# Performance work log

Hardware: AMD Instinct MI355X
Metric: run time of the kernel (lower is better)

The kernel has to match this reference:

```python
import jax, jax.numpy as jnp
import numpy as np

DIM = 768
NUM_EXPERTS = 4
NUM_HEADS = 12
HEAD_DIM = DIM // NUM_HEADS
MLP_HID = 4 * DIM
FC1_OUT = MLP_HID + 3 * DIM   # 5376 (mlp hidden + qkv)
FC2_IN = MLP_HID + DIM        # 3840 (mlp hidden + attn out)
FC2_OUT = 2 * DIM             # 1536 (mlp out + attn proj out)
CAP_FACTOR = 0.5
LN_EPS = 1e-6


def setup_inputs() -> dict:
    key = jax.random.key(0)
    ks = jax.random.split(key, 4)
    B, N = 8, 1024
    return {
        "x": jax.random.normal(ks[0], (B, N, DIM), jnp.float32),
        "w_router": jax.random.normal(ks[1], (NUM_EXPERTS, DIM), jnp.float32) * 0.02,
        "gamma1": jnp.ones((DIM,), jnp.float32),
        "beta1": jnp.zeros((DIM,), jnp.float32),
        "w1": jax.random.normal(ks[2], (FC1_OUT, DIM), jnp.float32) * 0.02,
        "b1": jnp.zeros((FC1_OUT,), jnp.float32),
        "w2": jax.random.normal(ks[3], (FC2_OUT, FC2_IN), jnp.float32) * 0.02,
        "b2": jnp.zeros((FC2_OUT,), jnp.float32),
    }


def reference(x, w_router, gamma1, beta1, w1, b1, w2, b2):
    B, N, C = x.shape
    E = NUM_EXPERTS
    cap = int(CAP_FACTOR * N)
    # nested (MoNE) per-expert active dims: [96, 192, 384, 768] for E=4, C=768
    m = np.array([C // 2 ** (E - 1 - e) for e in range(E)])
    in_mask = (np.arange(C)[None, :] < m[:, None]).astype(np.float32)  # [E, C]
    in_mask = jnp.asarray(in_mask)
    out_mask = jnp.concatenate([in_mask, in_mask], axis=-1)  # [E, 2C] for fc2 chunks

    # ---- expert-choice router ----
    logits = jnp.einsum('bnc,ec->bne', x, w_router)          # [B, N, E]
    probs = jax.nn.softmax(logits, axis=-1)
    gate, idx = jax.lax.top_k(jnp.swapaxes(probs, 1, 2), cap)  # [B, E, cap]
    dispatch = jax.nn.one_hot(idx, N, dtype=x.dtype)           # [B, E, cap, N]
    combine = dispatch * gate[..., None]                       # [B, E, cap, N]

    # ---- norm1 ----
    mu = jnp.mean(x, -1, keepdims=True)
    var = jnp.var(x, -1, keepdims=True)
    y = (x - mu) * jax.lax.rsqrt(var + LN_EPS) * gamma1 + beta1

    # ---- experts_choose_masked_contract (fc1, nested input dims) ----
    xg = jnp.einsum('becn,bnd->becd', dispatch, y)             # gather [B,E,cap,C]
    xg = xg * in_mask[None, :, None, :]                        # nested expert slice
    h = jnp.einsum('becd,fd->becf', xg, w1) + b1               # [B,E,cap,FC1_OUT]
    h = jnp.einsum('becn,becf->bnf', dispatch, h)              # scatter [B,N,FC1_OUT]

    x_mlp, x_qkv = h[..., :MLP_HID], h[..., MLP_HID:]

    # ---- attention ----
    qkv = x_qkv.reshape(B, N, 3, NUM_HEADS, HEAD_DIM).transpose(2, 0, 3, 1, 4)
    q, k, v = qkv[0], qkv[1], qkv[2]                           # [B,H,N,hd]
    scale = HEAD_DIM ** -0.5
    attn = jax.nn.softmax(jnp.einsum('bhqd,bhkd->bhqk', q, k) * scale, axis=-1)
    x_attn = jnp.einsum('bhqk,bhkd->bhqd', attn, v)
    x_attn = x_attn.transpose(0, 2, 1, 3).reshape(B, N, C)

    # ---- mlp activation + concat ----
    x_mlp = jax.nn.gelu(x_mlp, approximate=False)
    y2 = jnp.concatenate([x_mlp, x_attn], axis=-1)             # [B,N,FC2_IN]

    # ---- experts_choose_masked_expand (fc2, nested output dims, combine-weighted) ----
    yg = jnp.einsum('becn,bnf->becf', dispatch, y2)            # gather [B,E,cap,FC2_IN]
    o = jnp.einsum('becf,of->beco', yg, w2) + b2               # [B,E,cap,FC2_OUT]
    o = o * out_mask[None, :, None, :]                         # nested expert output slice
    z = jnp.einsum('becn,beco->bno', combine, o)               # combine [B,N,FC2_OUT]

    x_mlp2, x_attn2 = z[..., :C], z[..., C:]
    return x + x_mlp2 + x_attn2
```

## Files before the change

### kernel.cpp

```cpp
#include <hip/hip_runtime.h>
#include <math.h>

typedef __bf16 bf16_t;
typedef __bf16 bf16x8 __attribute__((ext_vector_type(8)));
typedef __bf16 bf16x4 __attribute__((ext_vector_type(4)));
typedef float f32x4 __attribute__((ext_vector_type(4)));

#define DIM 768
#define NE 4
#define NH 12
#define HD 64
#define MLP_HID 3072
#define FC1_OUT 5376
#define FC2_IN 3840
#define CAP 512
#define LOG2E 1.44269504088896340736f

__device__ __forceinline__ void async_copy16(const void* g, void* l) {
  __builtin_amdgcn_global_load_lds((const __attribute__((address_space(1))) void*)g,
                                   (__attribute__((address_space(3))) void*)l, 16, 0, 0);
}

__device__ __forceinline__ float gelu_f(float v) {
  float v2 = v * v;
  float t = v * fmaf(-0.102944f, v2, -2.302208f);
  float e = exp2f(t);
  return v * __builtin_amdgcn_rcpf(1.0f + e);
}

__global__ __launch_bounds__(256) void cast_router_kernel(const float* __restrict__ w1,
                                                          const float* __restrict__ w2,
                                                          bf16_t* __restrict__ w1b,
                                                          bf16_t* __restrict__ w2b,
                                                          const float* __restrict__ x,
                                                          const float* __restrict__ wr,
                                                          float* __restrict__ probs) {
  if (blockIdx.x < 2048) {
    const int N1 = FC1_OUT * DIM / 4;
    const int N2 = 1536 * FC2_IN / 4;
    const float4* w1v = (const float4*)w1;
    const float4* w2v = (const float4*)w2;
    for (int i = blockIdx.x * 256 + threadIdx.x; i < N1 + N2; i += 2048 * 256) {
      float4 f;
      bf16_t* dst;
      if (i < N1) { f = w1v[i]; dst = w1b + (size_t)i * 4; }
      else        { f = w2v[i - N1]; dst = w2b + (size_t)(i - N1) * 4; }
      bf16x4 o;
      o[0] = (bf16_t)f.x; o[1] = (bf16_t)f.y; o[2] = (bf16_t)f.z; o[3] = (bf16_t)f.w;
      *(bf16x4*)dst = o;
    }
    return;
  }
  int t = (blockIdx.x - 2048) * 4 + (threadIdx.x >> 6);
  int l = threadIdx.x & 63;
  const float4* xr = (const float4*)(x + (size_t)t * DIM);
  const float4* wr4 = (const float4*)wr;
  float a0 = 0.f, a1 = 0.f, a2 = 0.f, a3 = 0.f;
#pragma unroll
  for (int i = 0; i < 3; i++) {
    int d4 = l + i * 64;
    float4 xv = xr[d4];
    float4 w0 = wr4[d4];
    float4 w1e = wr4[192 + d4];
    float4 w2e = wr4[384 + d4];
    float4 w3e = wr4[576 + d4];
    a0 += xv.x * w0.x + xv.y * w0.y + xv.z * w0.z + xv.w * w0.w;
    a1 += xv.x * w1e.x + xv.y * w1e.y + xv.z * w1e.z + xv.w * w1e.w;
    a2 += xv.x * w2e.x + xv.y * w2e.y + xv.z * w2e.z + xv.w * w2e.w;
    a3 += xv.x * w3e.x + xv.y * w3e.y + xv.z * w3e.z + xv.w * w3e.w;
  }
#pragma unroll
  for (int off = 32; off > 0; off >>= 1) {
    a0 += __shfl_down(a0, off);
    a1 += __shfl_down(a1, off);
    a2 += __shfl_down(a2, off);
    a3 += __shfl_down(a3, off);
  }
  if (l == 0) {
    float m = fmaxf(fmaxf(a0, a1), fmaxf(a2, a3));
    float e0 = expf(a0 - m), e1 = expf(a1 - m), e2 = expf(a2 - m), e3 = expf(a3 - m);
    float inv = 1.0f / (e0 + e1 + e2 + e3);
    int b = t >> 10, n = t & 1023;
    probs[(b * NE + 0) * 1024 + n] = e0 * inv;
    probs[(b * NE + 1) * 1024 + n] = e1 * inv;
    probs[(b * NE + 2) * 1024 + n] = e2 * inv;
    probs[(b * NE + 3) * 1024 + n] = e3 * inv;
  }
}

__global__ __launch_bounds__(256) void rank_kernel(const float* __restrict__ probs,
                                                   float* __restrict__ gate_tok) {
  int be = blockIdx.y;
  __shared__ float p[1024];
  for (int i = threadIdx.x; i < 1024; i += 256) p[i] = probs[be * 1024 + i];
  __syncthreads();
  int n = blockIdx.x * 256 + threadIdx.x;
  float pn = p[n];
  int rank = 0;
  for (int j = 0; j < 1024; j++) {
    float pj = p[j];
    rank += (pj > pn) || (pj == pn && j < n);
  }
  int b = be >> 2, e = be & 3;
  gate_tok[(size_t)((b << 10) + n) * 4 + e] = (rank < CAP) ? pn : 0.0f;
}

__global__ __launch_bounds__(256) void ln_kernel(const float* __restrict__ x,
                                                 const float* __restrict__ gamma,
                                                 const float* __restrict__ beta,
                                                 const float* __restrict__ gate_tok,
                                                 bf16_t* __restrict__ ytil,
                                                 float* __restrict__ cntf,
                                                 float* __restrict__ g4) {
  int t = blockIdx.x * 4 + (threadIdx.x >> 6);
  int l = threadIdx.x & 63;
  float4 gg = ((const float4*)gate_tok)[t];
  float s0 = (gg.x > 0.f) ? 1.f : 0.f;
  float s1 = (gg.y > 0.f) ? 1.f : 0.f;
  float s2 = (gg.z > 0.f) ? 1.f : 0.f;
  float s3 = (gg.w > 0.f) ? 1.f : 0.f;
  float c3 = s3, c2 = c3 + s2, c1 = c2 + s1, c0 = c1 + s0;
  if (l == 0) {
    cntf[t] = c0;
    float4 G;
    G.x = gg.x + gg.y + gg.z + gg.w;
    G.y = gg.y + gg.z + gg.w;
    G.z = gg.z + gg.w;
    G.w = gg.w;
    ((float4*)g4)[t] = G;
  }
  const float4* xr = (const float4*)(x + (size_t)t * DIM);
  const float4* gm4 = (const float4*)gamma;
  const float4* bt4 = (const float4*)beta;
  float4 v[3];
  float s = 0.f, sq = 0.f;
#pragma unroll
  for (int i = 0; i < 3; i++) {
    v[i] = xr[l + i * 64];
    s += v[i].x + v[i].y + v[i].z + v[i].w;
    sq += v[i].x * v[i].x + v[i].y * v[i].y + v[i].z * v[i].z + v[i].w * v[i].w;
  }
#pragma unroll
  for (int off = 1; off < 64; off <<= 1) {
    s += __shfl_xor(s, off);
    sq += __shfl_xor(sq, off);
  }
  float mean = s * (1.0f / DIM);
  float var = sq * (1.0f / DIM) - mean * mean;
  float rs = rsqrtf(var + 1e-6f);
#pragma unroll
  for (int i = 0; i < 3; i++) {
    int d4 = l + i * 64;
    int d0 = d4 * 4;
    float cf = (d0 < 96) ? c0 : (d0 < 192) ? c1 : (d0 < 384) ? c2 : c3;
    float4 gmv = gm4[d4], btv = bt4[d4];
    bf16x4 o;
    o[0] = (bf16_t)(((v[i].x - mean) * rs * gmv.x + btv.x) * cf);
    o[1] = (bf16_t)(((v[i].y - mean) * rs * gmv.y + btv.y) * cf);
    o[2] = (bf16_t)(((v[i].z - mean) * rs * gmv.z + btv.z) * cf);
    o[3] = (bf16_t)(((v[i].w - mean) * rs * gmv.w + btv.w) * cf);
    *(bf16x4*)(ytil + (size_t)t * DIM + d0) = o;
  }
}

__global__ __launch_bounds__(256, 4) void fc1_kernel(const bf16_t* __restrict__ ytil,
                                                     const bf16_t* __restrict__ w1b,
                                                     const float* __restrict__ b1,
                                                     const float* __restrict__ cntf,
                                                     bf16_t* __restrict__ y2b,
                                                     bf16_t* __restrict__ qb,
                                                     bf16_t* __restrict__ kb,
                                                     bf16_t* __restrict__ vtb) {
  const int bid = blockIdx.x;
  const int xcd = bid & 7, j = bid >> 3;
  const int mt = xcd * 8 + (j & 7);
  const int nt = j >> 3;
  const int tid = threadIdx.x;
  const int w = tid >> 6, l = tid & 63;
  const int lq = l >> 4, lr = l & 15;

  __shared__ __align__(16) bf16_t lA[128 * 64];
  __shared__ __align__(16) bf16_t lB[128 * 64];

  f32x4 acc[4][4] = {};
  const int mwave = (w & 1) * 64, nwave = (w >> 1) * 64;
  const int crow = l >> 3;
  const int cbg = (l & 7) ^ (crow & 7);

  for (int k0 = 0; k0 < DIM; k0 += 64) {
#pragma unroll
    for (int i = 0; i < 4; i++) {
      int c = w * 4 + i;
      int row = c * 8 + crow;
      async_copy16(ytil + (size_t)(mt * 128 + row) * DIM + k0 + cbg * 8, lA + c * 512);
      async_copy16(w1b + (size_t)(nt * 128 + row) * DIM + k0 + cbg * 8, lB + c * 512);
    }
    __syncthreads();
#pragma unroll
    for (int ks = 0; ks < 2; ks++) {
      const int cbA = ((ks * 4 + lq) ^ (lr & 7)) * 8;
      bf16x8 af[4], bfr[4];
#pragma unroll
      for (int mi = 0; mi < 4; mi++)
        af[mi] = *(const bf16x8*)(lA + (mwave + mi * 16 + lr) * 64 + cbA);
#pragma unroll
      for (int ni = 0; ni < 4; ni++)
        bfr[ni] = *(const bf16x8*)(lB + (nwave + ni * 16 + lr) * 64 + cbA);
#pragma unroll
      for (int mi = 0; mi < 4; mi++)
#pragma unroll
        for (int ni = 0; ni < 4; ni++)
          acc[mi][ni] = __builtin_amdgcn_mfma_f32_16x16x32_bf16(af[mi], bfr[ni], acc[mi][ni], 0, 0, 0);
    }
    __syncthreads();
  }

#pragma unroll
  for (int mi = 0; mi < 4; mi++) {
    int row0 = mt * 128 + mwave + mi * 16 + lq * 4;
    float cnt[4];
#pragma unroll
    for (int r = 0; r < 4; r++) cnt[r] = cntf[row0 + r];
#pragma unroll
    for (int ni = 0; ni < 4; ni++) {
      int col = nt * 128 + nwave + ni * 16 + lr;
      float bias = b1[col];
      if (col < MLP_HID) {
#pragma unroll
        for (int r = 0; r < 4; r++) {
          float v = acc[mi][ni][r] + cnt[r] * bias;
          y2b[(size_t)(row0 + r) * FC2_IN + col] = (bf16_t)gelu_f(v);
        }
      } else {
        int part = col - MLP_HID;
        int comp = (part >= 1536) ? 2 : (part >= 768) ? 1 : 0;
        int rem = part - comp * 768;
        int hh = rem >> 6, d = rem & 63;
        int b = row0 >> 10, n0 = row0 & 1023;
        size_t base = (size_t)(b * NH + hh);
        if (comp == 2) {
          bf16x4 pk;
#pragma unroll
          for (int r = 0; r < 4; r++)
            pk[r] = (bf16_t)(acc[mi][ni][r] + cnt[r] * bias);
          *(bf16x4*)(vtb + (base * HD + d) * 1024 + n0) = pk;
        } else {
#pragma unroll
          for (int r = 0; r < 4; r++) {
            float v = acc[mi][ni][r] + cnt[r] * bias;
            if (comp == 0) qb[(base * 1024 + n0 + r) * HD + d] = (bf16_t)(v * (0.125f * LOG2E));
            else           kb[(base * 1024 + n0 + r) * HD + d] = (bf16_t)v;
          }
        }
      }
    }
  }
}

__global__ __launch_bounds__(256) void attn_kernel(const bf16_t* __restrict__ qb,
                                                   const bf16_t* __restrict__ kb,
                                                   const bf16_t* __restrict__ vtb,
                                                   bf16_t* __restrict__ y2b) {
  const int bid = blockIdx.x;
  const int xcd = bid & 7, j = bid >> 3;
  const int bh = xcd * 12 + (j >> 3);
  const int qt = j & 7;
  const int tid = threadIdx.x;
  const int w = tid >> 6, l = tid & 63, lq = l >> 4, lr = l & 15;

  __shared__ __align__(16) bf16_t lK[64 * 64];
  __shared__ __align__(16) bf16_t lV[64 * 64];
  __shared__ __align__(16) bf16_t lP[4][16 * 72];

  const bf16_t* qbase = qb + (size_t)bh * 1024 * HD;
  const bf16_t* kbase = kb + (size_t)bh * 1024 * HD;
  const bf16_t* vbase = vtb + (size_t)bh * HD * 1024;

  bf16x8 qf[2][2];
#pragma unroll
  for (int h = 0; h < 2; h++) {
    int qrow = qt * 128 + h * 64 + w * 16 + lr;
#pragma unroll
    for (int s = 0; s < 2; s++)
      qf[h][s] = *(const bf16x8*)(qbase + (size_t)qrow * HD + s * 32 + lq * 8);
  }

  f32x4 oacc[2][4] = {};
  float psum[2][4] = {};

  const int crow = l >> 3;
  const int cbg = (l & 7) ^ (crow & 7);

  for (int kt = 0; kt < 16; kt++) {
#pragma unroll
    for (int i = 0; i < 2; i++) {
      int c = w * 2 + i;
      int row = c * 8 + crow;
      async_copy16(kbase + (size_t)(kt * 64 + row) * HD + cbg * 8, lK + c * 512);
      async_copy16(vbase + (size_t)row * 1024 + kt * 64 + cbg * 8, lV + c * 512);
    }
    __syncthreads();

#pragma unroll
    for (int h = 0; h < 2; h++) {
      f32x4 sacc[4] = {};
#pragma unroll
      for (int s = 0; s < 2; s++) {
        const int cb = ((s * 4 + lq) ^ (lr & 7)) * 8;
#pragma unroll
        for (int kbq = 0; kbq < 4; kbq++) {
          bf16x8 kf = *(const bf16x8*)(lK + (kbq * 16 + lr) * 64 + cb);
          sacc[kbq] = __builtin_amdgcn_mfma_f32_16x16x32_bf16(qf[h][s], kf, sacc[kbq], 0, 0, 0);
        }
      }

#pragma unroll
      for (int kbq = 0; kbq < 4; kbq++)
#pragma unroll
        for (int r = 0; r < 4; r++) {
          float pv = exp2f(sacc[kbq][r]);
          psum[h][r] += pv;
          lP[w][(lq * 4 + r) * 72 + kbq * 16 + lr] = (bf16_t)pv;
        }

      bf16x8 pf[2];
#pragma unroll
      for (int s = 0; s < 2; s++)
        pf[s] = *(const bf16x8*)(&lP[w][lr * 72 + s * 32 + lq * 8]);

#pragma unroll
      for (int s = 0; s < 2; s++) {
        const int cb = ((s * 4 + lq) ^ (lr & 7)) * 8;
#pragma unroll
        for (int nb = 0; nb < 4; nb++) {
          bf16x8 vf = *(const bf16x8*)(lV + (nb * 16 + lr) * 64 + cb);
          oacc[h][nb] = __builtin_amdgcn_mfma_f32_16x16x32_bf16(pf[s], vf, oacc[h][nb], 0, 0, 0);
        }
      }
    }
    __syncthreads();
  }

  int b = bh / NH, hh = bh % NH;
#pragma unroll
  for (int h = 0; h < 2; h++) {
#pragma unroll
    for (int off = 1; off < 16; off <<= 1)
#pragma unroll
      for (int r = 0; r < 4; r++) psum[h][r] += __shfl_xor(psum[h][r], off);
    float rinv[4];
#pragma unroll
    for (int r = 0; r < 4; r++) rinv[r] = 1.0f / psum[h][r];
#pragma unroll
    for (int nb = 0; nb < 4; nb++)
#pragma unroll
      for (int r = 0; r < 4; r++) {
        float v = oacc[h][nb][r] * rinv[r];
        int tok = qt * 128 + h * 64 + w * 16 + lq * 4 + r;
        y2b[((size_t)(b * 1024 + tok)) * FC2_IN + MLP_HID + hh * HD + nb * 16 + lr] = (bf16_t)v;
      }
  }
}

__global__ __launch_bounds__(256, 4) void fc2_kernel(const bf16_t* __restrict__ y2b,
                                                     const bf16_t* __restrict__ w2b,
                                                     const float* __restrict__ b2,
                                                     const float* __restrict__ g4,
                                                     const float* __restrict__ x,
                                                     float* __restrict__ out) {
  const int bid = blockIdx.x;
  const int xcd = bid & 7, j = bid >> 3;
  const int mt = xcd * 8 + j / 12;
  const int ct = j % 12;
  const int tid = threadIdx.x;
  const int w = tid >> 6, l = tid & 63;
  const int lq = l >> 4, lr = l & 15;

  __shared__ __align__(16) bf16_t lA[128 * 64];
  __shared__ __align__(16) bf16_t lB[128 * 64];

  f32x4 acc[2][4][2] = {};
  const int mwave = (w & 1) * 64, nwave = (w >> 1) * 32;
  const int crow = l >> 3;
  const int cbg = (l & 7) ^ (crow & 7);

  for (int k0 = 0; k0 < FC2_IN; k0 += 64) {
#pragma unroll
    for (int i = 0; i < 4; i++) {
      int c = w * 4 + i;
      int row = c * 8 + crow;
      async_copy16(y2b + (size_t)(mt * 128 + row) * FC2_IN + k0 + cbg * 8, lA + c * 512);
      int grow = ((row >> 6) * 768) + ct * 64 + (row & 63);
      async_copy16(w2b + (size_t)grow * FC2_IN + k0 + cbg * 8, lB + c * 512);
    }
    __syncthreads();
#pragma unroll
    for (int ks = 0; ks < 2; ks++) {
      const int cbA = ((ks * 4 + lq) ^ (lr & 7)) * 8;
      bf16x8 af[4], bfr[2][2];
#pragma unroll
      for (int mi = 0; mi < 4; mi++)
        af[mi] = *(const bf16x8*)(lA + (mwave + mi * 16 + lr) * 64 + cbA);
#pragma unroll
      for (int h = 0; h < 2; h++)
#pragma unroll
        for (int ni = 0; ni < 2; ni++)
          bfr[h][ni] = *(const bf16x8*)(lB + (h * 64 + nwave + ni * 16 + lr) * 64 + cbA);
#pragma unroll
      for (int h = 0; h < 2; h++)
#pragma unroll
        for (int mi = 0; mi < 4; mi++)
#pragma unroll
          for (int ni = 0; ni < 2; ni++)
            acc[h][mi][ni] = __builtin_amdgcn_mfma_f32_16x16x32_bf16(af[mi], bfr[h][ni], acc[h][mi][ni], 0, 0, 0);
    }
    __syncthreads();
  }

#pragma unroll
  for (int mi = 0; mi < 4; mi++) {
    int row0 = mt * 128 + mwave + mi * 16 + lq * 4;
    float4 G[4];
#pragma unroll
    for (int r = 0; r < 4; r++) G[r] = ((const float4*)g4)[row0 + r];
#pragma unroll
    for (int ni = 0; ni < 2; ni++) {
      int col = ct * 64 + nwave + ni * 16 + lr;
      float b20 = b2[col], b21 = b2[768 + col];
#pragma unroll
      for (int r = 0; r < 4; r++) {
        float gw = (col < 96) ? G[r].x : (col < 192) ? G[r].y : (col < 384) ? G[r].z : G[r].w;
        float o = (acc[0][mi][ni][r] + b20) + (acc[1][mi][ni][r] + b21);
        size_t idx = (size_t)(row0 + r) * DIM + col;
        out[idx] = x[idx] + gw * o;
      }
    }
  }
}

extern "C" void kernel_launch(void* const* d_in, const int* in_sizes, int n_in,
                              void* d_out, int out_size, void* d_ws, size_t ws_size,
                              hipStream_t stream) {
  const float* x     = (const float*)d_in[0];
  const float* wr    = (const float*)d_in[1];
  const float* gamma = (const float*)d_in[2];
  const float* beta  = (const float*)d_in[3];
  const float* w1    = (const float*)d_in[4];
  const float* b1    = (const float*)d_in[5];
  const float* w2    = (const float*)d_in[6];
  const float* b2    = (const float*)d_in[7];
  float* out = (float*)d_out;

  char* ws = (char*)d_ws;
  float*  probs    = (float*)(ws + 0);
  float*  gate_tok = (float*)(ws + 131072);
  float*  cntf     = (float*)(ws + 262144);
  float*  g4       = (float*)(ws + 294912);
  bf16_t* w1b      = (bf16_t*)(ws + 425984);
  bf16_t* w2b      = (bf16_t*)(ws + 8683520);
  bf16_t* ytil     = (bf16_t*)(ws + 20480000);
  bf16_t* y2b      = (bf16_t*)(ws + 33062912);
  bf16_t* qb       = (bf16_t*)(ws + 95977472);
  bf16_t* kb       = (bf16_t*)(ws + 108560384);
  bf16_t* vtb      = (bf16_t*)(ws + 121143296);

  cast_router_kernel<<<4096, 256, 0, stream>>>(w1, w2, w1b, w2b, x, wr, probs);
  rank_kernel<<<dim3(4, 32), 256, 0, stream>>>(probs, gate_tok);
  ln_kernel<<<2048, 256, 0, stream>>>(x, gamma, beta, gate_tok, ytil, cntf, g4);
  fc1_kernel<<<2688, 256, 0, stream>>>(ytil, w1b, b1, cntf, y2b, qb, kb, vtb);
  attn_kernel<<<768, 256, 0, stream>>>(qb, kb, vtb, y2b);
  fc2_kernel<<<768, 256, 0, stream>>>(y2b, w2b, b2, g4, x, out);
}
```

Before: 368.4 us.

## Swap MFMA operands for vectorized fc1 epilogue stores and double-buffer attention K/V

In the fc1 GEMM, tiles that feed the MLP and Q/K outputs swap the MFMA operand order. Each lane then holds four consecutive output columns for one token, so GELU and Q/K results can be written as packed bf16x4 stores with float4 bias loads instead of scattered scalar stores. V tiles keep the old layout for the transposed store. The attention kernel double-buffers its K/V LDS tiles, issuing the next tile's async load before computing on the current one. This overlaps global loads with MFMA work at the cost of twice the K/V shared memory.

```diff
diff --git a/kernel.cpp b/kernel.cpp
--- a/kernel.cpp
+++ b/kernel.cpp
@@ -186,6 +186,7 @@
   const int mwave = (w & 1) * 64, nwave = (w >> 1) * 64;
   const int crow = l >> 3;
   const int cbg = (l & 7) ^ (crow & 7);
+  const bool swp = (nt < 36);
 
   for (int k0 = 0; k0 < DIM; k0 += 64) {
 #pragma unroll
@@ -206,52 +207,86 @@
 #pragma unroll
       for (int ni = 0; ni < 4; ni++)
         bfr[ni] = *(const bf16x8*)(lB + (nwave + ni * 16 + lr) * 64 + cbA);
-#pragma unroll
-      for (int mi = 0; mi < 4; mi++)
-#pragma unroll
-        for (int ni = 0; ni < 4; ni++)
-          acc[mi][ni] = __builtin_amdgcn_mfma_f32_16x16x32_bf16(af[mi], bfr[ni], acc[mi][ni], 0, 0, 0);
+      if (swp) {
+#pragma unroll
+        for (int mi = 0; mi < 4; mi++)
+#pragma unroll
+          for (int ni = 0; ni < 4; ni++)
+            acc[mi][ni] = __builtin_amdgcn_mfma_f32_16x16x32_bf16(bfr[ni], af[mi], acc[mi][ni], 0, 0, 0);
+      } else {
+#pragma unroll
+        for (int mi = 0; mi < 4; mi++)
+#pragma unroll
+          for (int ni = 0; ni < 4; ni++)
+            acc[mi][ni] = __builtin_amdgcn_mfma_f32_16x16x32_bf16(af[mi], bfr[ni], acc[mi][ni], 0, 0, 0);
+      }
     }
     __syncthreads();
   }
 
-#pragma unroll
-  for (int mi = 0; mi < 4; mi++) {
-    int row0 = mt * 128 + mwave + mi * 16 + lq * 4;
-    float cnt[4];
-#pragma unroll
-    for (int r = 0; r < 4; r++) cnt[r] = cntf[row0 + r];
-#pragma unroll
-    for (int ni = 0; ni < 4; ni++) {
-      int col = nt * 128 + nwave + ni * 16 + lr;
-      float bias = b1[col];
-      if (col < MLP_HID) {
-#pragma unroll
-        for (int r = 0; r < 4; r++) {
-          float v = acc[mi][ni][r] + cnt[r] * bias;
-          y2b[(size_t)(row0 + r) * FC2_IN + col] = (bf16_t)gelu_f(v);
-        }
-      } else {
-        int part = col - MLP_HID;
-        int comp = (part >= 1536) ? 2 : (part >= 768) ? 1 : 0;
-        int rem = part - comp * 768;
+  if (nt < 24) {
+#pragma unroll
+    for (int mi = 0; mi < 4; mi++) {
+      int token = mt * 128 + mwave + mi * 16 + lr;
+      float cnt = cntf[token];
+#pragma unroll
+      for (int ni = 0; ni < 4; ni++) {
+        int col0 = nt * 128 + nwave + ni * 16 + lq * 4;
+        float4 bv = *(const float4*)(b1 + col0);
+        bf16x4 o;
+        o[0] = (bf16_t)gelu_f(acc[mi][ni][0] + cnt * bv.x);
+        o[1] = (bf16_t)gelu_f(acc[mi][ni][1] + cnt * bv.y);
+        o[2] = (bf16_t)gelu_f(acc[mi][ni][2] + cnt * bv.z);
+        o[3] = (bf16_t)gelu_f(acc[mi][ni][3] + cnt * bv.w);
+        *(bf16x4*)(y2b + (size_t)token * FC2_IN + col0) = o;
+      }
+    }
+  } else if (nt < 36) {
+    const int comp = (nt < 30) ? 0 : 1;
+    bf16_t* __restrict__ dst = (comp == 0) ? qb : kb;
+    const float qs = 0.125f * LOG2E;
+#pragma unroll
+    for (int mi = 0; mi < 4; mi++) {
+      int token = mt * 128 + mwave + mi * 16 + lr;
+      float cnt = cntf[token];
+      int b = token >> 10, n0 = token & 1023;
+#pragma unroll
+      for (int ni = 0; ni < 4; ni++) {
+        int col0 = nt * 128 + nwave + ni * 16 + lq * 4;
+        float4 bv = *(const float4*)(b1 + col0);
+        int rem = col0 - MLP_HID - comp * 768;
+        int hh = rem >> 6, d0 = rem & 63;
+        size_t base = (size_t)(b * NH + hh);
+        bf16x4 o;
+        float v0 = acc[mi][ni][0] + cnt * bv.x;
+        float v1 = acc[mi][ni][1] + cnt * bv.y;
+        float v2 = acc[mi][ni][2] + cnt * bv.z;
+        float v3 = acc[mi][ni][3] + cnt * bv.w;
+        if (comp == 0) { v0 *= qs; v1 *= qs; v2 *= qs; v3 *= qs; }
+        o[0] = (bf16_t)v0; o[1] = (bf16_t)v1; o[2] = (bf16_t)v2; o[3] = (bf16_t)v3;
+        *(bf16x4*)(dst + (base * 1024 + n0) * HD + d0) = o;
+      }
+    }
+  } else {
+#pragma unroll
+    for (int mi = 0; mi < 4; mi++) {
+      int row0 = mt * 128 + mwave + mi * 16 + lq * 4;
+      float cnt[4];
+#pragma unroll
+      for (int r = 0; r < 4; r++) cnt[r] = cntf[row0 + r];
+      int b = row0 >> 10, n0 = row0 & 1023;
+#pragma unroll
+      for (int ni = 0; ni < 4; ni++) {
+        int col = nt * 128 + nwave + ni * 16 + lr;
+        float bias = b1[col];
+        int rem = col - MLP_HID - 1536;
         int hh = rem >> 6, d = rem & 63;
-        int b = row0 >> 10, n0 = row0 & 1023;
         size_t base = (size_t)(b * NH + hh);
-        if (comp == 2) {
-          bf16x4 pk;
-#pragma unroll
-          for (int r = 0; r < 4; r++)
-            pk[r] = (bf16_t)(acc[mi][ni][r] + cnt[r] * bias);
-          *(bf16x4*)(vtb + (base * HD + d) * 1024 + n0) = pk;
-        } else {
-#pragma unroll
-          for (int r = 0; r < 4; r++) {
-            float v = acc[mi][ni][r] + cnt[r] * bias;
-            if (comp == 0) qb[(base * 1024 + n0 + r) * HD + d] = (bf16_t)(v * (0.125f * LOG2E));
-            else           kb[(base * 1024 + n0 + r) * HD + d] = (bf16_t)v;
-          }
-        }
+        bf16x4 pk;
+#pragma unroll
+        for (int r = 0; r < 4; r++)
+          pk[r] = (bf16_t)(acc[mi][ni][r] + cnt[r] * bias);
+        *(bf16x4*)(vtb + (base * HD + d) * 1024 + n0) = pk;
       }
     }
   }
@@ -268,8 +303,8 @@
   const int tid = threadIdx.x;
   const int w = tid >> 6, l = tid & 63, lq = l >> 4, lr = l & 15;
 
-  __shared__ __align__(16) bf16_t lK[64 * 64];
-  __shared__ __align__(16) bf16_t lV[64 * 64];
+  __shared__ __align__(16) bf16_t lK[2][64 * 64];
+  __shared__ __align__(16) bf16_t lV[2][64 * 64];
   __shared__ __align__(16) bf16_t lP[4][16 * 72];
 
   const bf16_t* qbase = qb + (size_t)bh * 1024 * HD;
@@ -291,15 +326,22 @@
   const int crow = l >> 3;
   const int cbg = (l & 7) ^ (crow & 7);
 
-  for (int kt = 0; kt < 16; kt++) {
+  auto stage = [&](int buf, int kt) {
 #pragma unroll
     for (int i = 0; i < 2; i++) {
       int c = w * 2 + i;
       int row = c * 8 + crow;
-      async_copy16(kbase + (size_t)(kt * 64 + row) * HD + cbg * 8, lK + c * 512);
-      async_copy16(vbase + (size_t)row * 1024 + kt * 64 + cbg * 8, lV + c * 512);
-    }
-    __syncthreads();
+      async_copy16(kbase + (size_t)(kt * 64 + row) * HD + cbg * 8, &lK[buf][c * 512]);
+      async_copy16(vbase + (size_t)row * 1024 + kt * 64 + cbg * 8, &lV[buf][c * 512]);
+    }
+  };
+
+  stage(0, 0);
+  __syncthreads();
+
+  int cur = 0;
+  for (int kt = 0; kt < 16; kt++) {
+    if (kt + 1 < 16) stage(cur ^ 1, kt + 1);
 
 #pragma unroll
     for (int h = 0; h < 2; h++) {
@@ -309,7 +351,7 @@
         const int cb = ((s * 4 + lq) ^ (lr & 7)) * 8;
 #pragma unroll
         for (int kbq = 0; kbq < 4; kbq++) {
-          bf16x8 kf = *(const bf16x8*)(lK + (kbq * 16 + lr) * 64 + cb);
+          bf16x8 kf = *(const bf16x8*)(&lK[cur][(kbq * 16 + lr) * 64 + cb]);
           sacc[kbq] = __builtin_amdgcn_mfma_f32_16x16x32_bf16(qf[h][s], kf, sacc[kbq], 0, 0, 0);
         }
       }
@@ -333,12 +375,13 @@
         const int cb = ((s * 4 + lq) ^ (lr & 7)) * 8;
 #pragma unroll
         for (int nb = 0; nb < 4; nb++) {
-          bf16x8 vf = *(const bf16x8*)(lV + (nb * 16 + lr) * 64 + cb);
+          bf16x8 vf = *(const bf16x8*)(&lV[cur][(nb * 16 + lr) * 64 + cb]);
           oacc[h][nb] = __builtin_amdgcn_mfma_f32_16x16x32_bf16(pf[s], vf, oacc[h][nb], 0, 0, 0);
         }
       }
     }
     __syncthreads();
+    cur ^= 1;
   }
 
   int b = bh / NH, hh = bh % NH;
```

Measured after the change: 985.4 us. +167.5%, slower.
